# Kernel tuning notes

Hardware: AMD Instinct MI355X
Metric: run time of the kernel (lower is better)

Reference implementation:

```python
import jax, jax.numpy as jnp
import numpy as np

B, S, D, H = 16, 1024, 512, 8
DH = D // H


def setup_inputs() -> dict:
    key = jax.random.key(0)
    ks = jax.random.split(key, 8)
    q = jax.random.normal(ks[0], (B, S, D), dtype=jnp.float32)
    k = jax.random.normal(ks[1], (B, S, D), dtype=jnp.float32)
    v = jax.random.normal(ks[2], (B, S, D), dtype=jnp.float32)
    # causal lower-triangular mask (1 = attend), broadcastable [1,1,S,S]
    mask = jnp.tril(jnp.ones((S, S), dtype=jnp.int32))[None, None]
    # xavier-uniform weights, zero biases (matches _reset_parameters)
    def xavier(rk, fan):
        lim = float(np.sqrt(6.0 / (fan + fan)))
        return jax.random.uniform(rk, (fan, fan), jnp.float32, -lim, lim)
    Wk = xavier(ks[3], D)
    Wv = xavier(ks[4], D)
    Wo = xavier(ks[5], D)
    bk = jnp.zeros((D,), jnp.float32)
    bv = jnp.zeros((D,), jnp.float32)
    bo = jnp.zeros((D,), jnp.float32)
    return {"q": q, "k": k, "v": v, "mask": mask,
            "Wk": Wk, "bk": bk, "Wv": Wv, "bv": bv, "Wo": Wo, "bo": bo,
            "zero_pad": 1}


def reference(q, k, v, mask, Wk, bk, Wv, bv, Wo, bo, zero_pad):
    # key_query_same=True: q and k both use key_linear
    def split_heads(x):  # [B,S,D] -> [B,H,S,DH]
        return x.reshape(B, S, H, DH).transpose(0, 2, 1, 3)

    qh = split_heads(q @ Wk.T + bk)
    kh = split_heads(k @ Wk.T + bk)
    vh = split_heads(v @ Wv.T + bv)

    scores = jnp.einsum('bhqd,bhkd->bhqk', qh, kh) / jnp.sqrt(jnp.float32(DH))
    scores = jnp.where(mask == 0, jnp.float32(-1e32), scores)
    attn = jax.nn.softmax(scores, axis=-1)
    if zero_pad:  # zero out attention of the first query position (simpleKT trick)
        attn = attn.at[:, :, 0, :].set(0.0)
    # dropout p=0.0 (eval) -> identity
    out = jnp.einsum('bhqk,bhkd->bhqd', attn, vh)  # [B,H,S,DH]
    concat = out.transpose(0, 2, 1, 3).reshape(B, S, D)
    return concat @ Wo.T + bo
```

## Files before the change

### kernel.cpp

```cpp
#include <hip/hip_runtime.h>
#include <hip/hip_bf16.h>
#include <math.h>


typedef __attribute__((ext_vector_type(4))) float f32x4;
typedef __attribute__((ext_vector_type(8))) short bf16x8;

__device__ __forceinline__ short f2bf(float f) {
    union { float f; unsigned u; } x; x.f = f;
    unsigned r = x.u + 0x7fffu + ((x.u >> 16) & 1u);
    return (short)(r >> 16);
}
__device__ __forceinline__ short bfscale(short s, float f) {
    union { float f; unsigned u; } x; x.u = ((unsigned)(unsigned short)s) << 16;
    return f2bf(x.f * f);
}

__device__ __forceinline__ void gload_lds16(const void* g, void* l) {
    __builtin_amdgcn_global_load_lds(
        (const __attribute__((address_space(1))) unsigned int*)g,
        (__attribute__((address_space(3))) unsigned int*)l, 16, 0, 0);
}

__global__ void cvt_w_kernel(const float* __restrict__ w0, const float* __restrict__ w1,
                             const float* __restrict__ w2,
                             short* __restrict__ o0, short* __restrict__ o1,
                             short* __restrict__ o2)
{
    int z = blockIdx.y;
    const float* src = z == 0 ? w0 : (z == 1 ? w1 : w2);
    short* dst = z == 0 ? o0 : (z == 1 ? o1 : o2);
    int i = (blockIdx.x * 256 + threadIdx.x) * 4;
    float4 f = *(const float4*)(src + i);
    short4 s;
    s.x = f2bf(f.x); s.y = f2bf(f.y); s.z = f2bf(f.z); s.w = f2bf(f.w);
    *(short4*)(dst + i) = s;
}

template<int IN_BF16, int SPLIT>
__device__ __forceinline__ void gemm_body(const void* __restrict__ Xv,
                                          const short* __restrict__ W,
                                          const float* __restrict__ bias,
                                          void* __restrict__ Out,
                                          int m0, int n0)
{
    constexpr int ASTR = IN_BF16 ? 64 : 72;
    __shared__ short As[128 * ASTR];
    __shared__ short Bs[128 * 64];
    int tid = threadIdx.x;
    int lane = tid & 63, w = tid >> 6;
    int wr = (w >> 1) * 64, wc = (w & 1) * 64;
    int fr = lane & 15, hi = lane >> 4;
    int lrow = lane >> 3;
    int gcol = ((lane & 7) ^ (lrow & 3)) * 8;
    int xsw = ((hi ^ (lane & 3)) * 8);
    f32x4 acc[4][4] = {};

    const float* Xf = (const float*)Xv;
    const short* Xb = (const short*)Xv;

    float4 pf[8];
    if (!IN_BF16) {
        #pragma unroll
        for (int p = 0; p < 8; ++p) {
            int e = (p * 256 + tid) * 4;
            pf[p] = *(const float4*)(Xf + (size_t)(m0 + (e >> 6)) * 512 + (e & 63));
        }
    }

    for (int k0 = 0; k0 < 512; k0 += 64) {
        __syncthreads();
        #pragma unroll
        for (int c = 0; c < 4; ++c) {
            int chunk = w * 4 + c;
            gload_lds16(W + (size_t)(n0 + chunk * 8 + lrow) * 512 + k0 + gcol,
                        &Bs[chunk * 512]);
        }
        if (IN_BF16) {
            #pragma unroll
            for (int c = 0; c < 4; ++c) {
                int chunk = w * 4 + c;
                gload_lds16(Xb + (size_t)(m0 + chunk * 8 + lrow) * 512 + k0 + gcol,
                            &As[chunk * 512]);
            }
        } else {
            #pragma unroll
            for (int p = 0; p < 8; ++p) {
                int e = (p * 256 + tid) * 4;
                short4 s;
                s.x = f2bf(pf[p].x); s.y = f2bf(pf[p].y);
                s.z = f2bf(pf[p].z); s.w = f2bf(pf[p].w);
                *(short4*)&As[(e >> 6) * ASTR + (e & 63)] = s;
            }
        }
        __syncthreads();
        if (!IN_BF16 && k0 + 64 < 512) {
            #pragma unroll
            for (int p = 0; p < 8; ++p) {
                int e = (p * 256 + tid) * 4;
                pf[p] = *(const float4*)(Xf + (size_t)(m0 + (e >> 6)) * 512 + k0 + 64 + (e & 63));
            }
        }
        #pragma unroll
        for (int ks = 0; ks < 2; ++ks) {
            bf16x8 a[4], b[4];
            #pragma unroll
            for (int i = 0; i < 4; ++i) {
                int row = wr + i * 16 + fr;
                a[i] = IN_BF16
                    ? *(const bf16x8*)&As[row * ASTR + ks * 32 + xsw]
                    : *(const bf16x8*)&As[row * ASTR + ks * 32 + hi * 8];
            }
            #pragma unroll
            for (int j = 0; j < 4; ++j)
                b[j] = *(const bf16x8*)&Bs[(wc + j * 16 + fr) * 64 + ks * 32 + xsw];
            #pragma unroll
            for (int i = 0; i < 4; ++i)
                #pragma unroll
                for (int j = 0; j < 4; ++j)
                    acc[i][j] = __builtin_amdgcn_mfma_f32_16x16x32_bf16(a[i], b[j], acc[i][j], 0, 0, 0);
        }
    }
    int row4 = (lane >> 4) * 4;
    #pragma unroll
    for (int i = 0; i < 4; ++i) {
        #pragma unroll
        for (int j = 0; j < 4; ++j) {
            int gn = n0 + wc + j * 16 + fr;
            float bb = bias[gn];
            #pragma unroll
            for (int r = 0; r < 4; ++r) {
                int gm = m0 + wr + i * 16 + row4 + r;
                float v = acc[i][j][r] + bb;
                if (SPLIT == 1) {
                    int bidx = gm >> 10, s = gm & 1023, hh = gn >> 6, dh = gn & 63;
                    ((short*)Out)[((((size_t)bidx * 8 + hh) * 1024) + s) * 64 + dh] = f2bf(v);
                } else if (SPLIT == 2) {
                    int bidx = gm >> 10, s = gm & 1023, hh = gn >> 6, dh = gn & 63;
                    ((short*)Out)[((((size_t)bidx * 8 + hh) * 64) + dh) * 1024 + s] = f2bf(v);
                } else {
                    ((float*)Out)[(size_t)gm * 512 + gn] = v;
                }
            }
        }
    }
}

__global__ __launch_bounds__(256, 3) void proj_qk_kernel(
    const float* __restrict__ q, const float* __restrict__ k,
    const short* __restrict__ wk, const float* __restrict__ bk,
    short* __restrict__ qh, short* __restrict__ kh)
{
    int d = blockIdx.x;
    int wg = (d & 7) * 128 + (d >> 3);
    int z = wg >> 9;
    int rem = wg & 511;
    gemm_body<0, 1>(z ? (const void*)k : (const void*)q, wk, bk,
                    z ? (void*)kh : (void*)qh,
                    (rem >> 2) * 128, (rem & 3) * 128);
}

__global__ __launch_bounds__(256, 3) void proj_v_kernel(
    const float* __restrict__ v, const short* __restrict__ wv,
    const float* __restrict__ bv, short* __restrict__ vh)
{
    int d = blockIdx.x;
    int wg = (d & 7) * 64 + (d >> 3);
    gemm_body<0, 2>(v, wv, bv, vh, (wg >> 2) * 128, (wg & 3) * 128);
}

__global__ __launch_bounds__(256, 3) void proj_o_kernel(
    const short* __restrict__ ob, const short* __restrict__ wo,
    const float* __restrict__ bo, float* __restrict__ out)
{
    int d = blockIdx.x;
    int wg = (d & 7) * 64 + (d >> 3);
    gemm_body<1, 0>(ob, wo, bo, out, (wg >> 2) * 128, (wg & 3) * 128);
}

__global__ __launch_bounds__(512, 2) void attn_kernel(
    const short* __restrict__ QH, const short* __restrict__ KH,
    const short* __restrict__ VT, short* __restrict__ O,
    const int* __restrict__ zp)
{
    __shared__ short Ks[64][72];
    __shared__ short Vt[64][72];
    __shared__ short Ps[8][16][76];
    int tid = threadIdx.x, lane = tid & 63, w = tid >> 6;
    int fr = lane & 15, hi = lane >> 4;
    int d = blockIdx.x;
    int bh = (d & 7) * 16 + ((d >> 3) & 15);
    int p = d >> 7;
    const size_t basebh = (size_t)bh << 16;
    const short* Kb = KH + basebh;
    const short* Vb = VT + basebh;
    int r0 = tid >> 3, c0 = (tid & 7) * 8;
    int zero = zp[0];
    int b = bh >> 3, h = bh & 7;
    const float csc = 0.125f * 1.44269504f;

    for (int which = 0; which < 2; ++which) {
        int qt = which ? 7 - p : p;
        int qrow0 = qt * 128 + w * 16;
        int qtop = qrow0 + 15;
        int nkt = 2 * qt + 2;

        bf16x8 aQ[2];
        {
            const short* qp = QH + basebh + (size_t)(qrow0 + fr) * 64 + hi * 8;
            bf16x8 q0 = *(const bf16x8*)qp;
            bf16x8 q1 = *(const bf16x8*)(qp + 32);
            #pragma unroll
            for (int j = 0; j < 8; ++j) {
                aQ[0][j] = bfscale(q0[j], csc);
                aQ[1][j] = bfscale(q1[j], csc);
            }
        }

        f32x4 oacc[4] = {};
        float lsum[4] = {0.f, 0.f, 0.f, 0.f};

        bf16x8 kA, vA;
        kA = *(const bf16x8*)(Kb + r0 * 64 + c0);
        vA = *(const bf16x8*)(Vb + (size_t)r0 * 1024 + c0);

        for (int kt = 0; kt < nkt; ++kt) {
            __syncthreads();
            *(bf16x8*)&Ks[r0][c0] = kA;
            *(bf16x8*)&Vt[r0][c0] = vA;
            __syncthreads();
            if (kt + 1 < nkt) {
                const short* kp = Kb + (kt + 1) * 4096;
                const short* vp = Vb + (kt + 1) * 64;
                kA = *(const bf16x8*)(kp + r0 * 64 + c0);
                vA = *(const bf16x8*)(vp + (size_t)r0 * 1024 + c0);
            }
            if (kt * 64 > qtop) continue;

            f32x4 sa[4] = {};
            #pragma unroll
            for (int kf = 0; kf < 4; ++kf)
                #pragma unroll
                for (int ks = 0; ks < 2; ++ks) {
                    bf16x8 kb = *(const bf16x8*)&Ks[kf * 16 + fr][ks * 32 + hi * 8];
                    sa[kf] = __builtin_amdgcn_mfma_f32_16x16x32_bf16(aQ[ks], kb, sa[kf], 0, 0, 0);
                }

            if (kt * 64 + 63 > qrow0) {
                #pragma unroll
                for (int kf = 0; kf < 4; ++kf) {
                    int gk = kt * 64 + kf * 16 + fr;
                    #pragma unroll
                    for (int r = 0; r < 4; ++r) {
                        float pv = exp2f(sa[kf][r]);
                        if (gk > qrow0 + hi * 4 + r) pv = 0.f;
                        lsum[r] += pv;
                        union { float f; unsigned u; } c; c.f = pv;
                        Ps[w][hi * 4 + r][kf * 16 + fr] = (short)(c.u >> 16);
                    }
                }
            } else {
                #pragma unroll
                for (int kf = 0; kf < 4; ++kf)
                    #pragma unroll
                    for (int r = 0; r < 4; ++r) {
                        float pv = exp2f(sa[kf][r]);
                        lsum[r] += pv;
                        union { float f; unsigned u; } c; c.f = pv;
                        Ps[w][hi * 4 + r][kf * 16 + fr] = (short)(c.u >> 16);
                    }
            }

            bf16x8 pa[2];
            pa[0] = *(const bf16x8*)&Ps[w][fr][hi * 8];
            pa[1] = *(const bf16x8*)&Ps[w][fr][32 + hi * 8];
            #pragma unroll
            for (int df = 0; df < 4; ++df)
                #pragma unroll
                for (int ks = 0; ks < 2; ++ks) {
                    bf16x8 vb = *(const bf16x8*)&Vt[df * 16 + fr][ks * 32 + hi * 8];
                    oacc[df] = __builtin_amdgcn_mfma_f32_16x16x32_bf16(pa[ks], vb, oacc[df], 0, 0, 0);
                }
        }

        float inv[4];
        #pragma unroll
        for (int r = 0; r < 4; ++r) {
            float rs = lsum[r];
            #pragma unroll
            for (int off = 1; off < 16; off <<= 1) rs += __shfl_xor(rs, off);
            inv[r] = 1.0f / rs;
        }
        #pragma unroll
        for (int df = 0; df < 4; ++df)
            #pragma unroll
            for (int r = 0; r < 4; ++r) {
                int gq = qrow0 + hi * 4 + r;
                float v = oacc[df][r] * inv[r];
                if (zero && gq == 0) v = 0.f;
                O[((size_t)(b * 1024 + gq)) * 512 + h * 64 + df * 16 + fr] = f2bf(v);
            }
    }
}

extern "C" void kernel_launch(void* const* d_in, const int* in_sizes, int n_in,
                              void* d_out, int out_size, void* d_ws, size_t ws_size,
                              hipStream_t stream)
{
    const float* q  = (const float*)d_in[0];
    const float* k  = (const float*)d_in[1];
    const float* v  = (const float*)d_in[2];
    const float* Wk = (const float*)d_in[4];
    const float* bk = (const float*)d_in[5];
    const float* Wv = (const float*)d_in[6];
    const float* bv = (const float*)d_in[7];
    const float* Wo = (const float*)d_in[8];
    const float* bo = (const float*)d_in[9];
    const int*   zp = (const int*)d_in[10];
    float* out = (float*)d_out;

    short* wkb = (short*)d_ws;
    short* wvb = wkb + 262144;
    short* wob = wvb + 262144;
    short* qh  = wob + 262144;
    short* kh  = qh + 8388608;
    short* vh  = kh + 8388608;
    short* ob  = vh + 8388608;

    cvt_w_kernel<<<dim3(256, 3, 1), 256, 0, stream>>>(Wk, Wv, Wo, wkb, wvb, wob);
    proj_qk_kernel<<<dim3(1024, 1, 1), 256, 0, stream>>>(q, k, wkb, bk, qh, kh);
    proj_v_kernel<<<dim3(512, 1, 1), 256, 0, stream>>>(v, wvb, bv, vh);
    attn_kernel<<<dim3(512, 1, 1), 512, 0, stream>>>(qh, kh, vh, ob, zp);
    proj_o_kernel<<<dim3(512, 1, 1), 256, 0, stream>>>(ob, wob, bo, out);
}
```

Baseline: 114.7 us.

## Double-buffer K/V tiles via direct global-to-LDS loads with XOR swizzle

The attention kernel now stages K and V tiles with global_load_lds straight into two LDS buffers, prefetching the next tile while computing on the current one. This replaces the register round-trip and cuts the per-iteration barriers from two to one. The padded LDS layout is swapped for an XOR-swizzled unpadded layout so the MFMA operand reads avoid bank conflicts. It doubles K/V LDS usage, which may lower occupancy, and relies on the swizzle matching the direct-load write pattern.

```diff
diff --git a/kernel.cpp b/kernel.cpp
--- a/kernel.cpp
+++ b/kernel.cpp
@@ -183,8 +183,8 @@
     const short* __restrict__ VT, short* __restrict__ O,
     const int* __restrict__ zp)
 {
-    __shared__ short Ks[64][72];
-    __shared__ short Vt[64][72];
+    __shared__ short Ks[2][64 * 64];
+    __shared__ short Vt[2][64 * 64];
     __shared__ short Ps[8][16][76];
     int tid = threadIdx.x, lane = tid & 63, w = tid >> 6;
     int fr = lane & 15, hi = lane >> 4;
@@ -194,10 +194,12 @@
     const size_t basebh = (size_t)bh << 16;
     const short* Kb = KH + basebh;
     const short* Vb = VT + basebh;
-    int r0 = tid >> 3, c0 = (tid & 7) * 8;
     int zero = zp[0];
     int b = bh >> 3, h = bh & 7;
     const float csc = 0.125f * 1.44269504f;
+    int lrow = lane >> 3;
+    int gcol = ((lane & 7) ^ (lrow & 3)) * 8;
+    int xsw = (hi ^ (fr & 3)) * 8;
 
     for (int which = 0; which < 2; ++which) {
         int qt = which ? 7 - p : p;
@@ -220,67 +222,65 @@
         f32x4 oacc[4] = {};
         float lsum[4] = {0.f, 0.f, 0.f, 0.f};
 
-        bf16x8 kA, vA;
-        kA = *(const bf16x8*)(Kb + r0 * 64 + c0);
-        vA = *(const bf16x8*)(Vb + (size_t)r0 * 1024 + c0);
+        gload_lds16(Kb + (size_t)(w * 8 + lrow) * 64 + gcol, &Ks[0][w * 512]);
+        gload_lds16(Vb + (size_t)(w * 8 + lrow) * 1024 + gcol, &Vt[0][w * 512]);
+        __syncthreads();
 
         for (int kt = 0; kt < nkt; ++kt) {
-            __syncthreads();
-            *(bf16x8*)&Ks[r0][c0] = kA;
-            *(bf16x8*)&Vt[r0][c0] = vA;
-            __syncthreads();
+            int cur = kt & 1;
             if (kt + 1 < nkt) {
-                const short* kp = Kb + (kt + 1) * 4096;
+                const short* kp = Kb + (size_t)(kt + 1) * 4096;
                 const short* vp = Vb + (kt + 1) * 64;
-                kA = *(const bf16x8*)(kp + r0 * 64 + c0);
-                vA = *(const bf16x8*)(vp + (size_t)r0 * 1024 + c0);
-            }
-            if (kt * 64 > qtop) continue;
-
-            f32x4 sa[4] = {};
-            #pragma unroll
-            for (int kf = 0; kf < 4; ++kf)
-                #pragma unroll
-                for (int ks = 0; ks < 2; ++ks) {
-                    bf16x8 kb = *(const bf16x8*)&Ks[kf * 16 + fr][ks * 32 + hi * 8];
-                    sa[kf] = __builtin_amdgcn_mfma_f32_16x16x32_bf16(aQ[ks], kb, sa[kf], 0, 0, 0);
-                }
-
-            if (kt * 64 + 63 > qrow0) {
-                #pragma unroll
-                for (int kf = 0; kf < 4; ++kf) {
-                    int gk = kt * 64 + kf * 16 + fr;
-                    #pragma unroll
-                    for (int r = 0; r < 4; ++r) {
-                        float pv = exp2f(sa[kf][r]);
-                        if (gk > qrow0 + hi * 4 + r) pv = 0.f;
-                        lsum[r] += pv;
-                        union { float f; unsigned u; } c; c.f = pv;
-                        Ps[w][hi * 4 + r][kf * 16 + fr] = (short)(c.u >> 16);
-                    }
-                }
-            } else {
+                gload_lds16(kp + (size_t)(w * 8 + lrow) * 64 + gcol, &Ks[cur ^ 1][w * 512]);
+                gload_lds16(vp + (size_t)(w * 8 + lrow) * 1024 + gcol, &Vt[cur ^ 1][w * 512]);
+            }
+            if (kt * 64 <= qtop) {
+                f32x4 sa[4] = {};
                 #pragma unroll
                 for (int kf = 0; kf < 4; ++kf)
                     #pragma unroll
-                    for (int r = 0; r < 4; ++r) {
-                        float pv = exp2f(sa[kf][r]);
-                        lsum[r] += pv;
-                        union { float f; unsigned u; } c; c.f = pv;
-                        Ps[w][hi * 4 + r][kf * 16 + fr] = (short)(c.u >> 16);
+                    for (int ks = 0; ks < 2; ++ks) {
+                        bf16x8 kb = *(const bf16x8*)&Ks[cur][(kf * 16 + fr) * 64 + ks * 32 + xsw];
+                        sa[kf] = __builtin_amdgcn_mfma_f32_16x16x32_bf16(aQ[ks], kb, sa[kf], 0, 0, 0);
                     }
-            }
-
-            bf16x8 pa[2];
-            pa[0] = *(const bf16x8*)&Ps[w][fr][hi * 8];
-            pa[1] = *(const bf16x8*)&Ps[w][fr][32 + hi * 8];
-            #pragma unroll
-            for (int df = 0; df < 4; ++df)
+
+                if (kt * 64 + 63 > qrow0) {
+                    #pragma unroll
+                    for (int kf = 0; kf < 4; ++kf) {
+                        int gk = kt * 64 + kf * 16 + fr;
+                        #pragma unroll
+                        for (int r = 0; r < 4; ++r) {
+                            float pv = exp2f(sa[kf][r]);
+                            if (gk > qrow0 + hi * 4 + r) pv = 0.f;
+                            lsum[r] += pv;
+                            union { float f; unsigned u; } c; c.f = pv;
+                            Ps[w][hi * 4 + r][kf * 16 + fr] = (short)(c.u >> 16);
+                        }
+                    }
+                } else {
+                    #pragma unroll
+                    for (int kf = 0; kf < 4; ++kf)
+                        #pragma unroll
+                        for (int r = 0; r < 4; ++r) {
+                            float pv = exp2f(sa[kf][r]);
+                            lsum[r] += pv;
+                            union { float f; unsigned u; } c; c.f = pv;
+                            Ps[w][hi * 4 + r][kf * 16 + fr] = (short)(c.u >> 16);
+                        }
+                }
+
+                bf16x8 pa[2];
+                pa[0] = *(const bf16x8*)&Ps[w][fr][hi * 8];
+                pa[1] = *(const bf16x8*)&Ps[w][fr][32 + hi * 8];
                 #pragma unroll
-                for (int ks = 0; ks < 2; ++ks) {
-                    bf16x8 vb = *(const bf16x8*)&Vt[df * 16 + fr][ks * 32 + hi * 8];
-                    oacc[df] = __builtin_amdgcn_mfma_f32_16x16x32_bf16(pa[ks], vb, oacc[df], 0, 0, 0);
-                }
+                for (int df = 0; df < 4; ++df)
+                    #pragma unroll
+                    for (int ks = 0; ks < 2; ++ks) {
+                        bf16x8 vb = *(const bf16x8*)&Vt[cur][(df * 16 + fr) * 64 + ks * 32 + xsw];
+                        oacc[df] = __builtin_amdgcn_mfma_f32_16x16x32_bf16(pa[ks], vb, oacc[df], 0, 0, 0);
+                    }
+            }
+            __syncthreads();
         }
 
         float inv[4];
@@ -300,6 +300,7 @@
                 if (zero && gq == 0) v = 0.f;
                 O[((size_t)(b * 1024 + gq)) * 512 + h * 64 + df * 16 + fr] = f2bf(v);
             }
+        __syncthreads();
     }
 }
 
```

Result: no change. 116.3 us (+1.4%).

## Double-buffer GEMM LDS tiles to overlap next-tile global loads with MFMA

Applied to the files above, without the earlier changes.

The projection GEMM now keeps two LDS buffers for the weight tile, and for the bf16 input path two for the activation tile as well. The next K-slice's global-to-LDS loads are issued before the current slice's MFMAs run, instead of loading and computing in strict sequence. Hand-placed s_waitcnt plus s_barrier and sched_barrier replace the two __syncthreads per iteration. This doubles LDS use for those tiles, which may lower occupancy, and the hand-written wait counts must match the number of outstanding loads.

```diff
diff --git a/kernel.cpp b/kernel.cpp
--- a/kernel.cpp
+++ b/kernel.cpp
@@ -45,8 +45,8 @@
                                           int m0, int n0)
 {
     constexpr int ASTR = IN_BF16 ? 64 : 72;
-    __shared__ short As[128 * ASTR];
-    __shared__ short Bs[128 * 64];
+    __shared__ short As[(IN_BF16 ? 2 : 1) * 128 * ASTR];
+    __shared__ short Bs[2 * 128 * 64];
     int tid = threadIdx.x;
     int lane = tid & 63, w = tid >> 6;
     int wr = (w >> 1) * 64, wc = (w & 1) * 64;
@@ -60,7 +60,20 @@
     const short* Xb = (const short*)Xv;
 
     float4 pf[8];
-    if (!IN_BF16) {
+    #pragma unroll
+    for (int c = 0; c < 4; ++c) {
+        int chunk = w * 4 + c;
+        gload_lds16(W + (size_t)(n0 + chunk * 8 + lrow) * 512 + gcol,
+                    &Bs[chunk * 512]);
+    }
+    if (IN_BF16) {
+        #pragma unroll
+        for (int c = 0; c < 4; ++c) {
+            int chunk = w * 4 + c;
+            gload_lds16(Xb + (size_t)(m0 + chunk * 8 + lrow) * 512 + gcol,
+                        &As[chunk * 512]);
+        }
+    } else {
         #pragma unroll
         for (int p = 0; p < 8; ++p) {
             int e = (p * 256 + tid) * 4;
@@ -68,22 +81,26 @@
         }
     }
 
-    for (int k0 = 0; k0 < 512; k0 += 64) {
-        __syncthreads();
-        #pragma unroll
-        for (int c = 0; c < 4; ++c) {
-            int chunk = w * 4 + c;
-            gload_lds16(W + (size_t)(n0 + chunk * 8 + lrow) * 512 + k0 + gcol,
-                        &Bs[chunk * 512]);
-        }
+    for (int k0 = 0, it = 0; k0 < 512; k0 += 64, ++it) {
+        int cur = it & 1;
         if (IN_BF16) {
-            #pragma unroll
-            for (int c = 0; c < 4; ++c) {
-                int chunk = w * 4 + c;
-                gload_lds16(Xb + (size_t)(m0 + chunk * 8 + lrow) * 512 + k0 + gcol,
-                            &As[chunk * 512]);
+            asm volatile("s_waitcnt vmcnt(0)" ::: "memory");
+            __builtin_amdgcn_s_barrier();
+            __builtin_amdgcn_sched_barrier(0);
+            if (k0 + 64 < 512) {
+                #pragma unroll
+                for (int c = 0; c < 4; ++c) {
+                    int chunk = w * 4 + c;
+                    gload_lds16(W + (size_t)(n0 + chunk * 8 + lrow) * 512 + k0 + 64 + gcol,
+                                &Bs[(cur ^ 1) * 8192 + chunk * 512]);
+                    gload_lds16(Xb + (size_t)(m0 + chunk * 8 + lrow) * 512 + k0 + 64 + gcol,
+                                &As[(cur ^ 1) * 8192 + chunk * 512]);
+                }
             }
         } else {
+            asm volatile("s_waitcnt vmcnt(8)" ::: "memory");
+            __builtin_amdgcn_s_barrier();
+            __builtin_amdgcn_sched_barrier(0);
             #pragma unroll
             for (int p = 0; p < 8; ++p) {
                 int e = (p * 256 + tid) * 4;
@@ -92,14 +109,22 @@
                 s.z = f2bf(pf[p].z); s.w = f2bf(pf[p].w);
                 *(short4*)&As[(e >> 6) * ASTR + (e & 63)] = s;
             }
-        }
-        __syncthreads();
-        if (!IN_BF16 && k0 + 64 < 512) {
-            #pragma unroll
-            for (int p = 0; p < 8; ++p) {
-                int e = (p * 256 + tid) * 4;
-                pf[p] = *(const float4*)(Xf + (size_t)(m0 + (e >> 6)) * 512 + k0 + 64 + (e & 63));
-            }
+            if (k0 + 64 < 512) {
+                #pragma unroll
+                for (int c = 0; c < 4; ++c) {
+                    int chunk = w * 4 + c;
+                    gload_lds16(W + (size_t)(n0 + chunk * 8 + lrow) * 512 + k0 + 64 + gcol,
+                                &Bs[(cur ^ 1) * 8192 + chunk * 512]);
+                }
+                #pragma unroll
+                for (int p = 0; p < 8; ++p) {
+                    int e = (p * 256 + tid) * 4;
+                    pf[p] = *(const float4*)(Xf + (size_t)(m0 + (e >> 6)) * 512 + k0 + 64 + (e & 63));
+                }
+            }
+            asm volatile("s_waitcnt lgkmcnt(0)" ::: "memory");
+            __builtin_amdgcn_s_barrier();
+            __builtin_amdgcn_sched_barrier(0);
         }
         #pragma unroll
         for (int ks = 0; ks < 2; ++ks) {
@@ -108,12 +133,12 @@
             for (int i = 0; i < 4; ++i) {
                 int row = wr + i * 16 + fr;
                 a[i] = IN_BF16
-                    ? *(const bf16x8*)&As[row * ASTR + ks * 32 + xsw]
+                    ? *(const bf16x8*)&As[cur * 8192 + row * ASTR + ks * 32 + xsw]
                     : *(const bf16x8*)&As[row * ASTR + ks * 32 + hi * 8];
             }
             #pragma unroll
             for (int j = 0; j < 4; ++j)
-                b[j] = *(const bf16x8*)&Bs[(wc + j * 16 + fr) * 64 + ks * 32 + xsw];
+                b[j] = *(const bf16x8*)&Bs[cur * 8192 + (wc + j * 16 + fr) * 64 + ks * 32 + xsw];
             #pragma unroll
             for (int i = 0; i < 4; ++i)
                 #pragma unroll
```

New measurement: 112.8 us, median of 2. No clear change (-1.6%).
